# Kernel optimization log

Measured on AMD Instinct MI355X. Metric: run time of the kernel, lower is better.

## Reference

```python
import jax, jax.numpy as jnp
import numpy as np

B, D, L, K = 4096, 1280, 16384, 64


def setup_inputs() -> dict:
    key = jax.random.key(0)
    k1, k2, k3, k4, k5 = jax.random.split(key, 5)
    scale_enc = 1.0 / np.sqrt(D)
    scale_dec = 1.0 / np.sqrt(L)
    return {
        "x_BD": jax.random.normal(k1, (B, D), dtype=jnp.float32),
        "pb_D": jax.random.normal(k2, (D,), dtype=jnp.float32) * 0.01,
        "W_enc": jax.random.normal(k3, (D, L), dtype=jnp.float32) * scale_enc,
        "lb_L": jax.random.normal(k4, (L,), dtype=jnp.float32) * 0.01,
        "W_dec": jax.random.normal(k5, (L, D), dtype=jnp.float32) * scale_dec,
    }


def topk_activation(x_BL, k):
    # lax.top_k over last dim, relu the values, scatter back into zeros
    tv_Bk, ti_Bk = jax.lax.top_k(x_BL, k)
    tv_Bk = jax.nn.relu(tv_Bk)
    b_B = jnp.arange(x_BL.shape[0])[:, None]
    return jnp.zeros_like(x_BL).at[b_B, ti_Bk].set(tv_Bk)


def reference(x_BD, pb_D, W_enc, lb_L, W_dec):
    # encode: shift by pre-bias, dense, add latent bias
    xshift_BD = x_BD - pb_D
    zpre_BL = xshift_BD @ W_enc + lb_L          # [B, L]
    # top-k sparse activation
    z_BL = topk_activation(zpre_BL, K)          # [B, L], only K nonzeros per row
    # decode: dense matmul over full L (the kernel-headroom target)
    xhat_BD = z_BL @ W_dec + pb_D               # [B, D]
    return (zpre_BL, z_BL, xhat_BD)
```

## Files before the change

kernel.cpp:

```cpp
#include <hip/hip_runtime.h>
#include <hip/hip_bf16.h>
#include <stdint.h>

#define B_SZ 4096
#define D_SZ 1280
#define L_SZ 16384
#define K_TOP 64
#define C_CAP 192
#define BAND 0.07f

typedef __attribute__((ext_vector_type(8))) short s16x8;
typedef __attribute__((ext_vector_type(4))) float f32x4;

#define GLOAD_LDS16(gp, lp)                                                          \
  __builtin_amdgcn_global_load_lds((const __attribute__((address_space(1))) void*)(gp), \
                                   (__attribute__((address_space(3))) void*)(lp), 16, 0, 0)

static __device__ __forceinline__ unsigned short f2bf(float f) {
  __hip_bfloat16 h = __float2bfloat16(f);
  return *reinterpret_cast<unsigned short*>(&h);
}
static __device__ __forceinline__ float bf2f(unsigned short u) {
  return __uint_as_float((unsigned)u << 16);
}
static __device__ __forceinline__ unsigned mkkey(float f) {
  const unsigned u = __float_as_uint(f);
  return (u & 0x80000000u) ? ~u : (u | 0x80000000u);
}
static __device__ __forceinline__ float unkey(unsigned k) {
  const unsigned u = (k & 0x80000000u) ? (k & 0x7fffffffu) : ~k;
  return __uint_as_float(u);
}

__global__ __launch_bounds__(256) void sae_prep(const float* __restrict__ x,
                                                const float* __restrict__ pb,
                                                const float* __restrict__ We,
                                                const float* __restrict__ Wd,
                                                unsigned short* __restrict__ A,
                                                float* __restrict__ xs,
                                                float* __restrict__ WT,
                                                unsigned short* __restrict__ WbT,
                                                unsigned short* __restrict__ Wdb,
                                                int* __restrict__ bk_cnt) {
  const int b = blockIdx.x, t = threadIdx.x;
  if (b < 5120) {
    __shared__ float tile[64][65];
    const int l0 = (b & 255) * 64, d0 = (b >> 8) * 64;
    const int c = t & 63, rg = t >> 6;
#pragma unroll
    for (int i = 0; i < 16; ++i) {
      const int row = i * 4 + rg;
      tile[row][c] = We[(size_t)(d0 + row) * L_SZ + l0 + c];
    }
    __syncthreads();
#pragma unroll
    for (int i = 0; i < 16; ++i) {
      const int row = i * 4 + rg;
      const float v = tile[c][row];
      const size_t o = (size_t)(l0 + row) * D_SZ + d0 + c;
      WT[o] = v;
      WbT[o] = f2bf(v);
    }
  } else if (b < 5120 + 4096) {
    const int r = b - 5120;
    const float* xr = x + (size_t)r * D_SZ;
    unsigned short* ar = A + (size_t)r * D_SZ;
    float* sr = xs + (size_t)r * D_SZ;
    for (int d = t; d < D_SZ; d += 256) {
      const float v = xr[d] - pb[d];
      ar[d] = f2bf(v);
      sr[d] = v;
    }
  } else if (b < 5120 + 4096 + 2048) {
    const int n4 = L_SZ * D_SZ / 4;
    for (int i = (b - 9216) * 256 + t; i < n4; i += 2048 * 256) {
      const float4 v = ((const float4*)Wd)[i];
      ushort4 o;
      o.x = f2bf(v.x); o.y = f2bf(v.y); o.z = f2bf(v.z); o.w = f2bf(v.w);
      ((ushort4*)Wdb)[i] = o;
    }
  } else {
    bk_cnt[(b - 11264) * 256 + t] = 0;
  }
}

#define SWZ(lin) ((lin) ^ ((((lin) >> 9) & 7) << 4))
#define A_LDS 0
#define B_LDS 65536
#define KBYTES (D_SZ * 2)

#define PH_MID()                                          \
  __builtin_amdgcn_s_barrier();                           \
  asm volatile("s_waitcnt lgkmcnt(0)" ::: "memory");      \
  __builtin_amdgcn_sched_barrier(0);                      \
  __builtin_amdgcn_s_setprio(1)

#define PH_END()                                          \
  __builtin_amdgcn_s_setprio(0);                          \
  __builtin_amdgcn_s_barrier();                           \
  __builtin_amdgcn_sched_barrier(0)

__global__ __launch_bounds__(512, 2) void sae_gemm(const unsigned short* __restrict__ A,
                                                   const unsigned short* __restrict__ WT,
                                                   const float* __restrict__ lb,
                                                   float* __restrict__ zpre) {
  __shared__ short lds[65536];
  char* ldsc = (char*)lds;
  const int t = threadIdx.x, lane = t & 63, w = t >> 6;
  const int wr = w >> 2, wc = w & 3, w2 = w * 2;

  const int bid = blockIdx.x;
  const int xcd = bid & 7, i2 = bid >> 3;
  const int b2 = i2 >> 4, inner = i2 & 15;
  const int mt = (b2 & 3) * 4 + (inner & 3);
  const int nt = xcd * 8 + (b2 >> 2) * 4 + (inner >> 2);
  const int m0 = mt * 256, n0 = nt * 256;

  f32x4 acc[8][4] = {};

  auto STAGE = [&](const unsigned short* op, int rowbase, int ldsop, int buf, int half, int tile) {
#pragma unroll
    for (int s = 0; s < 2; ++s) {
      const int o = (w2 + s) * 1024 + lane * 16;
      const int r = o >> 7;
      const int cb = (o & 127) ^ (((o >> 9) & 7) << 4);
      const char* g = (const char*)op + (size_t)(rowbase + half * 128 + r) * KBYTES +
                      tile * 128 + cb;
      char* l = ldsc + ldsop + buf * 32768 + half * 16384 + (w2 + s) * 1024;
      GLOAD_LDS16(g, l);
    }
  };
  auto LDA = [&](s16x8* af, int buf, int q) {
#pragma unroll
    for (int i = 0; i < 2; ++i)
#pragma unroll
      for (int kk = 0; kk < 2; ++kk) {
        const int r = (q * 2 + i) * 16 + (lane & 15);
        int lin = r * 128 + kk * 64 + ((lane >> 4) * 16);
        lin = SWZ(lin);
        af[i * 2 + kk] = *(const s16x8*)(ldsc + A_LDS + buf * 32768 + wr * 16384 + lin);
      }
  };
  auto LDB = [&](s16x8* bg, int buf) {
#pragma unroll
    for (int j = 0; j < 4; ++j)
#pragma unroll
      for (int kk = 0; kk < 2; ++kk) {
        const int nloc = wc * 64 + j * 16 + (lane & 15);
        const int half = nloc >> 7, r = nloc & 127;
        int lin = r * 128 + kk * 64 + ((lane >> 4) * 16);
        lin = SWZ(lin);
        bg[j * 2 + kk] = *(const s16x8*)(ldsc + B_LDS + buf * 32768 + half * 16384 + lin);
      }
  };
  auto MM = [&](s16x8* af, s16x8* bg, int q) {
#pragma unroll
    for (int i = 0; i < 2; ++i)
#pragma unroll
      for (int j = 0; j < 4; ++j)
#pragma unroll
        for (int kk = 0; kk < 2; ++kk)
          acc[q * 2 + i][j] =
              __builtin_amdgcn_mfma_f32_16x16x32_bf16(af[i * 2 + kk], bg[j * 2 + kk],
                                                      acc[q * 2 + i][j], 0, 0, 0);
  };

  STAGE(WT, n0, B_LDS, 0, 0, 0); STAGE(WT, n0, B_LDS, 0, 1, 0);
  STAGE(A, m0, A_LDS, 0, 0, 0);  STAGE(A, m0, A_LDS, 0, 1, 0);
  STAGE(WT, n0, B_LDS, 1, 0, 1); STAGE(WT, n0, B_LDS, 1, 1, 1);
  asm volatile("s_waitcnt vmcnt(4)" ::: "memory");
  __builtin_amdgcn_s_barrier();
  __builtin_amdgcn_sched_barrier(0);

  const int NI = D_SZ / 128;
  for (int i = 0; i < NI; ++i) {
    const bool last = (i == NI - 1);
    s16x8 af[4], bg[8];
    LDB(bg, 0); LDA(af, 0, 0);
    STAGE(A, m0, A_LDS, 1, 0, 2 * i + 1); STAGE(A, m0, A_LDS, 1, 1, 2 * i + 1);
    PH_MID(); MM(af, bg, 0); PH_END();
    LDA(af, 0, 1);
    if (!last) STAGE(WT, n0, B_LDS, 0, 0, 2 * i + 2);
    PH_MID(); MM(af, bg, 1); PH_END();
    LDA(af, 0, 2);
    if (!last) STAGE(WT, n0, B_LDS, 0, 1, 2 * i + 2);
    PH_MID(); MM(af, bg, 2); PH_END();
    LDA(af, 0, 3);
    PH_MID(); MM(af, bg, 3);
    __builtin_amdgcn_s_setprio(0);
    if (last) { asm volatile("s_waitcnt vmcnt(0)" ::: "memory"); }
    else      { asm volatile("s_waitcnt vmcnt(4)" ::: "memory"); }
    __builtin_amdgcn_s_barrier();
    __builtin_amdgcn_sched_barrier(0);
    LDB(bg, 1); LDA(af, 1, 0);
    if (!last) STAGE(A, m0, A_LDS, 0, 0, 2 * i + 2);
    PH_MID(); MM(af, bg, 0); PH_END();
    LDA(af, 1, 1);
    if (!last) STAGE(A, m0, A_LDS, 0, 1, 2 * i + 2);
    PH_MID(); MM(af, bg, 1); PH_END();
    LDA(af, 1, 2);
    if (!last) STAGE(WT, n0, B_LDS, 1, 0, 2 * i + 3);
    PH_MID(); MM(af, bg, 2); PH_END();
    LDA(af, 1, 3);
    if (!last) STAGE(WT, n0, B_LDS, 1, 1, 2 * i + 3);
    PH_MID(); MM(af, bg, 3);
    __builtin_amdgcn_s_setprio(0);
    asm volatile("s_waitcnt vmcnt(4)" ::: "memory");
    __builtin_amdgcn_s_barrier();
    __builtin_amdgcn_sched_barrier(0);
  }

  const int cl = lane & 15, rg = lane >> 4;
#pragma unroll
  for (int j = 0; j < 4; ++j) {
    const int cc = n0 + wc * 64 + j * 16 + cl;
    const float bias = lb[cc];
#pragma unroll
    for (int i = 0; i < 8; ++i) {
      const size_t base = (size_t)(m0 + wr * 128 + i * 16 + rg * 4) * L_SZ + cc;
#pragma unroll
      for (int tt = 0; tt < 4; ++tt) zpre[base + (size_t)tt * L_SZ] = acc[i][j][tt] + bias;
    }
  }
}

__device__ void radix_pick(unsigned* hist, unsigned* suf, int* sh_b, unsigned* sh_above,
                           int target, int t) {
  if (t == 0) *sh_b = -1;
  unsigned p = hist[4 * t] + hist[4 * t + 1] + hist[4 * t + 2] + hist[4 * t + 3];
  suf[t] = p;
  for (int off = 1; off < 256; off <<= 1) {
    __syncthreads();
    unsigned v = (t + off < 256) ? suf[t + off] : 0u;
    __syncthreads();
    suf[t] += v;
  }
  __syncthreads();
  const unsigned shi = (t + 1 < 256) ? suf[t + 1] : 0u;
  unsigned S = shi;
  int best = -1;
#pragma unroll
  for (int i = 3; i >= 0; --i) {
    S += hist[4 * t + i];
    if (S >= (unsigned)target) { best = 4 * t + i; break; }
  }
  if (best >= 0) atomicMax(sh_b, best);
  __syncthreads();
  const int b = *sh_b;
  if ((b >> 2) == t) {
    unsigned above = shi;
    for (int i = 3; i > (b & 3); --i) above += hist[4 * t + i];
    *sh_above = above;
  }
  __syncthreads();
}

__device__ void radix_pick512(unsigned* hist, unsigned* suf, int* sh_b, unsigned* sh_above,
                              int target, int t) {
  if (t == 0) *sh_b = -1;
  if (t < 256) suf[t] = hist[4 * t] + hist[4 * t + 1] + hist[4 * t + 2] + hist[4 * t + 3];
  for (int off = 1; off < 256; off <<= 1) {
    __syncthreads();
    unsigned v = (t < 256 && t + off < 256) ? suf[t + off] : 0u;
    __syncthreads();
    if (t < 256) suf[t] += v;
  }
  __syncthreads();
  if (t < 256) {
    const unsigned shi = (t + 1 < 256) ? suf[t + 1] : 0u;
    unsigned S = shi;
    int best = -1;
#pragma unroll
    for (int i = 3; i >= 0; --i) {
      S += hist[4 * t + i];
      if (S >= (unsigned)target) { best = 4 * t + i; break; }
    }
    if (best >= 0) atomicMax(sh_b, best);
  }
  __syncthreads();
  const int b = *sh_b;
  if (t < 256 && (b >> 2) == t) {
    unsigned above = (t + 1 < 256) ? suf[t + 1] : 0u;
    for (int i = 3; i > (b & 3); --i) above += hist[4 * t + i];
    *sh_above = above;
  }
  __syncthreads();
}

__global__ __launch_bounds__(512) void sae_mega(const float* __restrict__ zpre,
                                                const float* __restrict__ xs,
                                                const float* __restrict__ WT,
                                                const float* __restrict__ lb,
                                                const unsigned short* __restrict__ Wdb,
                                                const float* __restrict__ pb,
                                                float* __restrict__ z,
                                                float* __restrict__ xhat) {
  __shared__ float row[L_SZ];
  __shared__ unsigned hist[1024];
  __shared__ unsigned suf[256];
  __shared__ int sh_b0, sh_b1, sh_nhi, sh_nband;
  __shared__ unsigned sh_above;
  __shared__ int bl[C_CAP];
  __shared__ float bfv[C_CAP];
  __shared__ double be[C_CAP];
  __shared__ int ids[K_TOP];
  __shared__ float vs[K_TOP];

  const int r = blockIdx.x, t = threadIdx.x, lane = t & 63, w = t >> 6;
  const float4* zr4 = (const float4*)(zpre + (size_t)r * L_SZ);

  float4 xc[5];
  {
    const float4* xr4 = (const float4*)(xs + (size_t)r * D_SZ);
#pragma unroll
    for (int i = 0; i < 5; ++i) xc[i] = xr4[lane + 64 * i];
  }

  for (int i = t; i < 1024; i += 512) hist[i] = 0;
  if (t == 0) { sh_nhi = 0; sh_nband = 0; }
  __syncthreads();
  for (int i = t; i < L_SZ / 4; i += 512) {
    const float4 v = zr4[i];
    ((float4*)row)[i] = v;
    atomicAdd(&hist[mkkey(v.x) >> 22], 1u);
    atomicAdd(&hist[mkkey(v.y) >> 22], 1u);
    atomicAdd(&hist[mkkey(v.z) >> 22], 1u);
    atomicAdd(&hist[mkkey(v.w) >> 22], 1u);
  }
  __syncthreads();
  radix_pick512(hist, suf, &sh_b0, &sh_above, K_TOP, t);
  const int b0 = sh_b0;
  const int target2 = K_TOP - (int)sh_above;
  __syncthreads();
  for (int i = t; i < 1024; i += 512) hist[i] = 0;
  __syncthreads();
  for (int i = t; i < L_SZ; i += 512) {
    const unsigned k = mkkey(row[i]);
    if ((int)(k >> 22) == b0) atomicAdd(&hist[(k >> 12) & 1023u], 1u);
  }
  __syncthreads();
  radix_pick512(hist, suf, &sh_b1, &sh_above, target2, t);
  const unsigned v64lb_key = (((unsigned)b0 << 10) | (unsigned)sh_b1) << 12;
  const float lo_f = unkey(v64lb_key) - BAND;
  const float hi_f = unkey(v64lb_key + 4095u) + BAND;
  __syncthreads();
  for (int i = t; i < L_SZ; i += 512) {
    const float val = row[i];
    if (val >= lo_f) {
      if (val > hi_f) {
        const int p = atomicAdd(&sh_nhi, 1);
        if (p < K_TOP) { ids[p] = i; vs[p] = fmaxf(val, 0.f); }
      } else {
        const int p = atomicAdd(&sh_nband, 1);
        if (p < C_CAP) { bl[p] = i; bfv[p] = val; }
      }
    }
  }
  __syncthreads();
  const int nh = sh_nhi < K_TOP ? sh_nhi : K_TOP;
  const int nb = sh_nband < C_CAP ? sh_nband : C_CAP;
  for (int e = w; e < nb; e += 8) {
    const int l = bl[e];
    const float4* wr4 = (const float4*)(WT + (size_t)l * D_SZ);
    double acc = 0.0;
#pragma unroll
    for (int i = 0; i < 5; ++i) {
      const float4 wv = wr4[lane + 64 * i];
      acc += (double)xc[i].x * (double)wv.x + (double)xc[i].y * (double)wv.y +
             (double)xc[i].z * (double)wv.z + (double)xc[i].w * (double)wv.w;
    }
#pragma unroll
    for (int off = 32; off > 0; off >>= 1) acc += __shfl_down(acc, off);
    if (lane == 0) be[e] = acc + (double)lb[l];
  }
  __syncthreads();
  const int need = K_TOP - nh;
  if (t < nb) {
    const double ev = be[t];
    const int l = bl[t];
    int rank = 0;
    for (int j = 0; j < nb; ++j) {
      const double e2 = be[j];
      if (e2 > ev || (e2 == ev && bl[j] < l)) ++rank;
    }
    if (rank < need) {
      ids[nh + rank] = l;
      vs[nh + rank] = fmaxf(bfv[t], 0.f);
    }
  }
  __syncthreads();
  if (t < 320) {
    float4 acc = ((const float4*)pb)[t];
#pragma unroll 8
    for (int k = 0; k < K_TOP; ++k) {
      const ushort4 wv = ((const ushort4*)(Wdb + (size_t)ids[k] * D_SZ))[t];
      const float vk = vs[k];
      acc.x += vk * bf2f(wv.x);
      acc.y += vk * bf2f(wv.y);
      acc.z += vk * bf2f(wv.z);
      acc.w += vk * bf2f(wv.w);
    }
    ((float4*)(xhat + (size_t)r * D_SZ))[t] = acc;
  } else {
    const int tz = t - 320;
    float4* zr = (float4*)(z + (size_t)r * L_SZ);
    for (int i = tz; i < L_SZ / 4; i += 192) zr[i] = make_float4(0.f, 0.f, 0.f, 0.f);
  }
  __syncthreads();
  if (t < K_TOP) z[(size_t)r * L_SZ + ids[t]] = vs[t];
}

__global__ __launch_bounds__(256) void sae_topc(const float* __restrict__ zpre,
                                                int* __restrict__ bk_cnt,
                                                int* __restrict__ band_lat,
                                                float* __restrict__ band_fval,
                                                int* __restrict__ n_hi,
                                                int* __restrict__ n_band,
                                                int* __restrict__ t_idx,
                                                float* __restrict__ t_val) {
  __shared__ unsigned hist[1024];
  __shared__ unsigned suf[256];
  __shared__ int sh_b0, sh_b1, sh_nhi, sh_nband;
  __shared__ unsigned sh_above;
  const int r = blockIdx.x, t = threadIdx.x;
  const float4* zr4 = (const float4*)(zpre + (size_t)r * L_SZ);

  for (int i = t; i < 1024; i += 256) hist[i] = 0;
  if (t == 0) { sh_nhi = 0; sh_nband = 0; }
  __syncthreads();
  for (int i = t; i < L_SZ / 4; i += 256) {
    const float4 v = zr4[i];
    atomicAdd(&hist[mkkey(v.x) >> 22], 1u);
    atomicAdd(&hist[mkkey(v.y) >> 22], 1u);
    atomicAdd(&hist[mkkey(v.z) >> 22], 1u);
    atomicAdd(&hist[mkkey(v.w) >> 22], 1u);
  }
  __syncthreads();
  radix_pick(hist, suf, &sh_b0, &sh_above, K_TOP, t);
  const int b0 = sh_b0;
  const int target2 = K_TOP - (int)sh_above;
  __syncthreads();
  for (int i = t; i < 1024; i += 256) hist[i] = 0;
  __syncthreads();
  for (int i = t; i < L_SZ / 4; i += 256) {
    const float4 v = zr4[i];
    const float va[4] = {v.x, v.y, v.z, v.w};
#pragma unroll
    for (int q = 0; q < 4; ++q) {
      const unsigned k = mkkey(va[q]);
      if ((int)(k >> 22) == b0) atomicAdd(&hist[(k >> 12) & 1023u], 1u);
    }
  }
  __syncthreads();
  radix_pick(hist, suf, &sh_b1, &sh_above, target2, t);
  const unsigned v64lb_key = (((unsigned)b0 << 10) | (unsigned)sh_b1) << 12;
  const float lo_f = unkey(v64lb_key) - BAND;
  const float hi_f = unkey(v64lb_key + 4095u) + BAND;
  __syncthreads();
  for (int i = t; i < L_SZ / 4; i += 256) {
    const float4 v = zr4[i];
    const float va[4] = {v.x, v.y, v.z, v.w};
#pragma unroll
    for (int q = 0; q < 4; ++q) {
      const float val = va[q];
      if (val >= lo_f) {
        const int l = 4 * i + q;
        if (val > hi_f) {
          const int p = atomicAdd(&sh_nhi, 1);
          if (p < K_TOP) {
            t_idx[(size_t)r * K_TOP + p] = l;
            t_val[(size_t)r * K_TOP + p] = fmaxf(val, 0.f);
          }
        } else {
          const int p = atomicAdd(&sh_nband, 1);
          if (p < C_CAP) {
            band_lat[(r << 8) + p] = l;
            band_fval[(r << 8) + p] = val;
            atomicAdd(&bk_cnt[l], 1);
          }
        }
      }
    }
  }
  __syncthreads();
  if (t == 0) {
    n_hi[r] = sh_nhi < K_TOP ? sh_nhi : K_TOP;
    n_band[r] = sh_nband < C_CAP ? sh_nband : C_CAP;
  }
}

__global__ __launch_bounds__(256) void sae_scan(const int* __restrict__ counts,
                                                int* __restrict__ offsets,
                                                int* __restrict__ cursor) {
  __shared__ int part[256];
  const int t = threadIdx.x;
  int s = 0;
  for (int i = 0; i < 64; ++i) s += counts[t * 64 + i];
  part[t] = s;
  __syncthreads();
  int excl = 0;
  for (int j = 0; j < t; ++j) excl += part[j];
  int run = excl;
  for (int i = 0; i < 64; ++i) {
    const int idx = t * 64 + i;
    offsets[idx] = run;
    cursor[idx] = run;
    run += counts[idx];
  }
}

__global__ __launch_bounds__(192) void sae_bucket_fill(const int* __restrict__ band_lat,
                                                       const int* __restrict__ n_band,
                                                       int* __restrict__ cursor,
                                                       int* __restrict__ entries) {
  const int r = blockIdx.x, t = threadIdx.x;
  if (t < n_band[r]) {
    const int l = band_lat[(r << 8) + t];
    const int pos = atomicAdd(&cursor[l], 1);
    entries[pos] = (r << 8) | t;
  }
}

__global__ __launch_bounds__(256) void sae_refine_lm(const float* __restrict__ xs,
                                                     const float* __restrict__ WT,
                                                     const float* __restrict__ lb,
                                                     const int* __restrict__ counts,
                                                     const int* __restrict__ offsets,
                                                     const int* __restrict__ entries,
                                                     double* __restrict__ band_eval) {
  __shared__ float4 wl[D_SZ / 4];
  const int l = blockIdx.x;
  const int t = threadIdx.x, lane = t & 63, w = t >> 6;
  const int n = counts[l];
  if (n == 0) return;
  const float4* wc = (const float4*)(WT + (size_t)l * D_SZ);
  for (int d = t; d < D_SZ / 4; d += 256) wl[d] = wc[d];
  __syncthreads();
  const int base = offsets[l];
  const double bias = (double)lb[l];
  for (int e = w; e < n; e += 4) {
    const int ent = entries[base + e];
    const int rr = ent >> 8;
    const float4* xr = (const float4*)(xs + (size_t)rr * D_SZ);
    double acc = 0.0;
#pragma unroll
    for (int i = 0; i < 5; ++i) {
      const float4 xv = xr[lane + 64 * i];
      const float4 wv = wl[lane + 64 * i];
      acc += (double)xv.x * (double)wv.x + (double)xv.y * (double)wv.y +
             (double)xv.z * (double)wv.z + (double)xv.w * (double)wv.w;
    }
#pragma unroll
    for (int off = 32; off > 0; off >>= 1) acc += __shfl_down(acc, off);
    if (lane == 0) band_eval[ent] = acc + bias;
  }
}

__global__ __launch_bounds__(320) void sae_finish_nz(const int* __restrict__ n_hi,
                                                     const int* __restrict__ n_band,
                                                     const int* __restrict__ band_lat,
                                                     const float* __restrict__ band_fval,
                                                     const double* __restrict__ band_eval,
                                                     int* __restrict__ t_idx,
                                                     float* __restrict__ t_val,
                                                     const unsigned short* __restrict__ Wdb,
                                                     const float* __restrict__ pb,
                                                     float* __restrict__ xhat) {
  __shared__ int bl[C_CAP];
  __shared__ float bf[C_CAP];
  __shared__ double be[C_CAP];
  __shared__ int ids[K_TOP];
  __shared__ float vs[K_TOP];
  const int r = blockIdx.x, t = threadIdx.x;
  const int nh = n_hi[r], nb = n_band[r];
  if (t < nb) {
    bl[t] = band_lat[(r << 8) + t];
    bf[t] = band_fval[(r << 8) + t];
    be[t] = band_eval[(r << 8) + t];
  }
  if (t < nh) {
    ids[t] = t_idx[(size_t)r * K_TOP + t];
    vs[t] = t_val[(size_t)r * K_TOP + t];
  }
  __syncthreads();
  const int need = K_TOP - nh;
  if (t < nb) {
    const double ev = be[t];
    const int l = bl[t];
    int rank = 0;
    for (int j = 0; j < nb; ++j) {
      const double e2 = be[j];
      if (e2 > ev || (e2 == ev && bl[j] < l)) ++rank;
    }
    if (rank < need) {
      const float fv = fmaxf(bf[t], 0.f);
      ids[nh + rank] = l;
      vs[nh + rank] = fv;
      t_idx[(size_t)r * K_TOP + nh + rank] = l;
      t_val[(size_t)r * K_TOP + nh + rank] = fv;
    }
  }
  __syncthreads();
  float4 acc = ((const float4*)pb)[t];
#pragma unroll 8
  for (int k = 0; k < K_TOP; ++k) {
    const ushort4 wv = ((const ushort4*)(Wdb + (size_t)ids[k] * D_SZ))[t];
    const float vk = vs[k];
    acc.x += vk * bf2f(wv.x);
    acc.y += vk * bf2f(wv.y);
    acc.z += vk * bf2f(wv.z);
    acc.w += vk * bf2f(wv.w);
  }
  ((float4*)(xhat + (size_t)r * D_SZ))[t] = acc;
}

__global__ void sae_scatterA(const int* __restrict__ top_idx, const float* __restrict__ top_val,
                             float* __restrict__ z) {
  const int r = blockIdx.x;
  const int t = threadIdx.x;
  const int id = top_idx[(size_t)r * K_TOP + t];
  const float v = top_val[(size_t)r * K_TOP + t];
  z[(size_t)r * L_SZ + id] = v;
}

__global__ __launch_bounds__(256) void sae_scatterB(const int* __restrict__ top_idx,
                                                    const float* __restrict__ top_val,
                                                    float* __restrict__ z) {
  __shared__ int ids[32 * K_TOP];
  __shared__ float vs[32 * K_TOP];
  const int t = threadIdx.x;
  for (int i = t; i < 32 * K_TOP; i += 256) {
    ids[i] = top_idx[(size_t)4064 * K_TOP + i];
    vs[i] = top_val[(size_t)4064 * K_TOP + i];
  }
  __syncthreads();
  float4* zz = (float4*)(z + (size_t)4064 * L_SZ);
  for (int i = t; i < 32 * L_SZ / 4; i += 256) zz[i] = make_float4(0.f, 0.f, 0.f, 0.f);
  __syncthreads();
  for (int i = t; i < 32 * K_TOP; i += 256) {
    const int rr = 4064 + i / K_TOP;
    z[(size_t)rr * L_SZ + ids[i]] = vs[i];
  }
}

extern "C" void kernel_launch(void* const* d_in, const int* in_sizes, int n_in,
                              void* d_out, int out_size, void* d_ws, size_t ws_size,
                              hipStream_t stream) {
  const float* x  = (const float*)d_in[0];
  const float* pb = (const float*)d_in[1];
  const float* We = (const float*)d_in[2];
  const float* lb = (const float*)d_in[3];
  const float* Wd = (const float*)d_in[4];

  float* zpre = (float*)d_out;
  float* z    = zpre + (size_t)B_SZ * L_SZ;
  float* xhat = z + (size_t)B_SZ * L_SZ;

  const bool use_ws = ws_size >= ((size_t)234 << 20);
  char* sb = use_ws ? (char*)d_ws : (char*)z;

  unsigned short* A_bf   = (unsigned short*)(sb);
  unsigned short* WT_bf  = (unsigned short*)(sb + ((size_t)16 << 20));
  float*          WT_f32 = (float*)(sb + ((size_t)64 << 20));
  float*          xs_f32 = (float*)(sb + ((size_t)144 << 20));
  int*            b_lat  = (int*)(sb + ((size_t)164 << 20));
  float*          b_fval = (float*)(sb + ((size_t)168 << 20));
  double*         b_eval = (double*)(sb + ((size_t)172 << 20));
  int*            bk_cnt = (int*)(sb + ((size_t)180 << 20));
  int*            bk_off = (int*)(sb + ((size_t)181 << 20));
  int*            bk_cur = (int*)(sb + ((size_t)182 << 20));
  int*            bk_ent = (int*)(sb + ((size_t)184 << 20));
  unsigned short* Wd_bf  = (unsigned short*)(sb + ((size_t)188 << 20));
  int*            nhi_g  = (int*)(sb + ((size_t)228 << 20));
  int*            nbd_g  = (int*)(sb + ((size_t)229 << 20));
  int*   t_idx = use_ws ? (int*)(sb + ((size_t)230 << 20))
                        : (int*)((char*)z + ((size_t)254 << 20));
  float* t_val = use_ws ? (float*)(sb + ((size_t)232 << 20))
                        : (float*)((char*)z + ((size_t)255 << 20));

  sae_prep<<<11328, 256, 0, stream>>>(x, pb, We, Wd, A_bf, xs_f32, WT_f32, WT_bf, Wd_bf, bk_cnt);
  sae_gemm<<<1024, 512, 0, stream>>>(A_bf, WT_bf, lb, zpre);
  if (use_ws) {
    sae_mega<<<B_SZ, 512, 0, stream>>>(zpre, xs_f32, WT_f32, lb, Wd_bf, pb, z, xhat);
  } else {
    sae_topc<<<B_SZ, 256, 0, stream>>>(zpre, bk_cnt, b_lat, b_fval, nhi_g, nbd_g, t_idx, t_val);
    sae_scan<<<1, 256, 0, stream>>>(bk_cnt, bk_off, bk_cur);
    sae_bucket_fill<<<B_SZ, 192, 0, stream>>>(b_lat, nbd_g, bk_cur, bk_ent);
    sae_refine_lm<<<L_SZ, 256, 0, stream>>>(xs_f32, WT_f32, lb, bk_cnt, bk_off, bk_ent, b_eval);
    sae_finish_nz<<<B_SZ, 320, 0, stream>>>(nhi_g, nbd_g, b_lat, b_fval, b_eval, t_idx, t_val,
                                            Wd_bf, pb, xhat);
    hipMemsetAsync(z, 0, (size_t)4064 * L_SZ * sizeof(float), stream);
    sae_scatterA<<<4064, K_TOP, 0, stream>>>(t_idx, t_val, z);
    sae_scatterB<<<1, 256, 0, stream>>>(t_idx, t_val, z);
  }
}
```

Before: 673.4 us.

## Prefilter top-k candidates by fixed threshold into compact LDS list

Replaces the full-row LDS copy and two full-row radix histogram passes with a single pass that collects elements above a fixed value threshold into a compact candidate list. The list is built with wave-ballot appends. The radix selection then runs only over this list, and a full-histogram fallback covers rows where the threshold catches too few or too many candidates. Histograms are also split four ways by lane to reduce LDS atomic contention. The cost is extra fallback logic and a data-dependent threshold that relies on the value distribution; it cuts LDS footprint and per-row selection work.

```diff
diff --git a/kernel.cpp b/kernel.cpp
--- a/kernel.cpp
+++ b/kernel.cpp
@@ -8,6 +8,8 @@
 #define K_TOP 64
 #define C_CAP 192
 #define BAND 0.07f
+#define LIST_CAP 4096
+#define T_COLLECT 1.5f
 
 typedef __attribute__((ext_vector_type(8))) short s16x8;
 typedef __attribute__((ext_vector_type(4))) float f32x4;
@@ -255,10 +257,17 @@
   __syncthreads();
 }
 
-__device__ void radix_pick512(unsigned* hist, unsigned* suf, int* sh_b, unsigned* sh_above,
-                              int target, int t) {
+__device__ void radix_pick4(unsigned* hist4, unsigned* suf, int* sh_b, unsigned* sh_above,
+                            int target, int t) {
   if (t == 0) *sh_b = -1;
-  if (t < 256) suf[t] = hist[4 * t] + hist[4 * t + 1] + hist[4 * t + 2] + hist[4 * t + 3];
+  if (t < 256) {
+    unsigned p = 0;
+#pragma unroll
+    for (int i = 0; i < 4; ++i)
+#pragma unroll
+      for (int c = 0; c < 4; ++c) p += hist4[(4 * t + i) * 4 + c];
+    suf[t] = p;
+  }
   for (int off = 1; off < 256; off <<= 1) {
     __syncthreads();
     unsigned v = (t < 256 && t + off < 256) ? suf[t + off] : 0u;
@@ -270,9 +279,11 @@
     const unsigned shi = (t + 1 < 256) ? suf[t + 1] : 0u;
     unsigned S = shi;
     int best = -1;
-#pragma unroll
     for (int i = 3; i >= 0; --i) {
-      S += hist[4 * t + i];
+      unsigned cnt = 0;
+#pragma unroll
+      for (int c = 0; c < 4; ++c) cnt += hist4[(4 * t + i) * 4 + c];
+      S += cnt;
       if (S >= (unsigned)target) { best = 4 * t + i; break; }
     }
     if (best >= 0) atomicMax(sh_b, best);
@@ -281,7 +292,12 @@
   const int b = *sh_b;
   if (t < 256 && (b >> 2) == t) {
     unsigned above = (t + 1 < 256) ? suf[t + 1] : 0u;
-    for (int i = 3; i > (b & 3); --i) above += hist[4 * t + i];
+    for (int i = 3; i > (b & 3); --i) {
+      unsigned cnt = 0;
+#pragma unroll
+      for (int c = 0; c < 4; ++c) cnt += hist4[(4 * t + i) * 4 + c];
+      above += cnt;
+    }
     *sh_above = above;
   }
   __syncthreads();
@@ -295,10 +311,11 @@
                                                 const float* __restrict__ pb,
                                                 float* __restrict__ z,
                                                 float* __restrict__ xhat) {
-  __shared__ float row[L_SZ];
-  __shared__ unsigned hist[1024];
+  __shared__ unsigned hist4[4096];
   __shared__ unsigned suf[256];
-  __shared__ int sh_b0, sh_b1, sh_nhi, sh_nband;
+  __shared__ int l_idx[LIST_CAP];
+  __shared__ unsigned l_key[LIST_CAP];
+  __shared__ int sh_n, sh_b0, sh_b1, sh_nhi, sh_nband;
   __shared__ unsigned sh_above;
   __shared__ int bl[C_CAP];
   __shared__ float bfv[C_CAP];
@@ -316,43 +333,99 @@
     for (int i = 0; i < 5; ++i) xc[i] = xr4[lane + 64 * i];
   }
 
-  for (int i = t; i < 1024; i += 512) hist[i] = 0;
-  if (t == 0) { sh_nhi = 0; sh_nband = 0; }
-  __syncthreads();
+  auto push = [&](int idx, unsigned k, bool pred) {
+    const unsigned long long m = __ballot(pred);
+    if (!m) return;
+    const int leader = (int)__ffsll((long long)m) - 1;
+    int base = 0;
+    if (lane == leader) base = atomicAdd(&sh_n, (int)__popcll(m));
+    base = __shfl(base, leader);
+    if (pred) {
+      const int pos = base + (int)__popcll(m & ((1ull << lane) - 1ull));
+      if (pos < LIST_CAP) { l_idx[pos] = idx; l_key[pos] = k; }
+    }
+  };
+
+  if (t == 0) { sh_n = 0; sh_nhi = 0; sh_nband = 0; }
+  __syncthreads();
+  const unsigned keyT = mkkey(T_COLLECT);
   for (int i = t; i < L_SZ / 4; i += 512) {
     const float4 v = zr4[i];
-    ((float4*)row)[i] = v;
-    atomicAdd(&hist[mkkey(v.x) >> 22], 1u);
-    atomicAdd(&hist[mkkey(v.y) >> 22], 1u);
-    atomicAdd(&hist[mkkey(v.z) >> 22], 1u);
-    atomicAdd(&hist[mkkey(v.w) >> 22], 1u);
-  }
-  __syncthreads();
-  radix_pick512(hist, suf, &sh_b0, &sh_above, K_TOP, t);
-  const int b0 = sh_b0;
-  const int target2 = K_TOP - (int)sh_above;
-  __syncthreads();
-  for (int i = t; i < 1024; i += 512) hist[i] = 0;
-  __syncthreads();
-  for (int i = t; i < L_SZ; i += 512) {
-    const unsigned k = mkkey(row[i]);
-    if ((int)(k >> 22) == b0) atomicAdd(&hist[(k >> 12) & 1023u], 1u);
-  }
-  __syncthreads();
-  radix_pick512(hist, suf, &sh_b1, &sh_above, target2, t);
-  const unsigned v64lb_key = (((unsigned)b0 << 10) | (unsigned)sh_b1) << 12;
-  const float lo_f = unkey(v64lb_key) - BAND;
-  const float hi_f = unkey(v64lb_key + 4095u) + BAND;
-  __syncthreads();
-  for (int i = t; i < L_SZ; i += 512) {
-    const float val = row[i];
+    const float va[4] = {v.x, v.y, v.z, v.w};
+#pragma unroll
+    for (int q = 0; q < 4; ++q) {
+      const unsigned k = mkkey(va[q]);
+      push(4 * i + q, k, k >= keyT);
+    }
+  }
+  __syncthreads();
+  int nlist = sh_n < LIST_CAP ? sh_n : LIST_CAP;
+  bool need_full = (sh_n < K_TOP) || (sh_n > LIST_CAP);
+  float thresh_val = T_COLLECT;
+  float lo_f = 0.f, hi_f = 0.f;
+
+  for (int attempt = 0; attempt < 2; ++attempt) {
+    if (need_full) {
+      for (int i = t; i < 4096; i += 512) hist4[i] = 0;
+      __syncthreads();
+      for (int i = t; i < L_SZ / 4; i += 512) {
+        const float4 v = zr4[i];
+        const float va[4] = {v.x, v.y, v.z, v.w};
+#pragma unroll
+        for (int q = 0; q < 4; ++q)
+          atomicAdd(&hist4[(mkkey(va[q]) >> 22) * 4 + (lane & 3)], 1u);
+      }
+      __syncthreads();
+      radix_pick4(hist4, suf, &sh_b0, &sh_above, K_TOP, t);
+      const int cb0 = sh_b0;
+      const unsigned lt = (unsigned)(cb0 > 8 ? cb0 - 8 : 0) << 22;
+      thresh_val = unkey(lt);
+      if (t == 0) sh_n = 0;
+      __syncthreads();
+      for (int i = t; i < L_SZ / 4; i += 512) {
+        const float4 v = zr4[i];
+        const float va[4] = {v.x, v.y, v.z, v.w};
+#pragma unroll
+        for (int q = 0; q < 4; ++q) {
+          const unsigned k = mkkey(va[q]);
+          push(4 * i + q, k, k >= lt);
+        }
+      }
+      __syncthreads();
+      nlist = sh_n < LIST_CAP ? sh_n : LIST_CAP;
+    }
+    for (int i = t; i < 4096; i += 512) hist4[i] = 0;
+    __syncthreads();
+    for (int i = t; i < nlist; i += 512)
+      atomicAdd(&hist4[(l_key[i] >> 22) * 4 + (lane & 3)], 1u);
+    __syncthreads();
+    radix_pick4(hist4, suf, &sh_b0, &sh_above, K_TOP, t);
+    const int b0 = sh_b0;
+    const int tgt2 = K_TOP - (int)sh_above;
+    for (int i = t; i < 4096; i += 512) hist4[i] = 0;
+    __syncthreads();
+    for (int i = t; i < nlist; i += 512) {
+      const unsigned k = l_key[i];
+      if ((int)(k >> 22) == b0) atomicAdd(&hist4[((k >> 12) & 1023u) * 4 + (lane & 3)], 1u);
+    }
+    __syncthreads();
+    radix_pick4(hist4, suf, &sh_b1, &sh_above, tgt2, t);
+    const unsigned v64lb_key = (((unsigned)b0 << 10) | (unsigned)sh_b1) << 12;
+    lo_f = unkey(v64lb_key) - BAND;
+    hi_f = unkey(v64lb_key + 4095u) + BAND;
+    if (thresh_val <= lo_f) break;
+    need_full = true;
+  }
+
+  for (int i = t; i < nlist; i += 512) {
+    const float val = unkey(l_key[i]);
     if (val >= lo_f) {
       if (val > hi_f) {
         const int p = atomicAdd(&sh_nhi, 1);
-        if (p < K_TOP) { ids[p] = i; vs[p] = fmaxf(val, 0.f); }
+        if (p < K_TOP) { ids[p] = l_idx[i]; vs[p] = fmaxf(val, 0.f); }
       } else {
         const int p = atomicAdd(&sh_nband, 1);
-        if (p < C_CAP) { bl[p] = i; bfv[p] = val; }
+        if (p < C_CAP) { bl[p] = l_idx[i]; bfv[p] = val; }
       }
     }
   }
```

New measurement: 667.3 us. No clear change (-0.9%).
